# Optimization experiments

Measured on AMD Instinct MI355X. Metric: run time of the kernel, lower is better.

The kernel has to match this reference:

```python
import jax, jax.numpy as jnp
import numpy as np
import math

B, S, D, H = 4, 1024, 1024, 16
HD = D // H  # 64
DFF = 4 * D
LN_EPS = 1e-5

def setup_inputs() -> dict:
    key = jax.random.key(0)
    ks = jax.random.split(key, 24)
    sd = lambda fi, fo: 1.0 / math.sqrt(fi)
    def lin(k, fi, fo):
        k1, k2 = jax.random.split(k)
        w = jax.random.uniform(k1, (fi, fo), jnp.float32, -sd(fi, fo), sd(fi, fo))
        b = jax.random.uniform(k2, (fo,), jnp.float32, -sd(fi, fo), sd(fi, fo))
        return w, b
    x = jax.random.normal(ks[0], (B, S, D), jnp.float32)
    Wk, bk = lin(ks[1], D, D)
    Wq, bq = lin(ks[2], D, D)
    Wv, bv = lin(ks[3], D, D)
    # per-head projections stacked over heads: [H, D, HD]
    def head_lin(k):
        kk = jax.random.split(k, H)
        ws, bs = zip(*[lin(kk[h], D, HD) for h in range(H)])
        return jnp.stack(ws), jnp.stack(bs)
    Whq, bhq = head_lin(ks[4])
    Whk, bhk = head_lin(ks[5])
    Whv, bhv = head_lin(ks[6])
    Wo, bo = lin(ks[7], D, D)
    W1, b1 = lin(ks[8], D, DFF)
    W2, b2 = lin(ks[9], DFF, D)
    gamma = jnp.ones((D,), jnp.float32)
    beta = jnp.zeros((D,), jnp.float32)
    return dict(x=x, Wk=Wk, bk=bk, Wq=Wq, bq=bq, Wv=Wv, bv=bv,
                Whq=Whq, bhq=bhq, Whk=Whk, bhk=bhk, Whv=Whv, bhv=bhv,
                Wo=Wo, bo=bo, W1=W1, b1=b1, W2=W2, b2=b2,
                gamma=gamma, beta=beta)

def _layer_norm(x, gamma, beta):
    mu = jnp.mean(x, axis=-1, keepdims=True)
    var = jnp.mean(jnp.square(x - mu), axis=-1, keepdims=True)
    return (x - mu) * jax.lax.rsqrt(var + LN_EPS) * gamma + beta

def reference(x, Wk, bk, Wq, bq, Wv, bv, Whq, bhq, Whk, bhk, Whv, bhv,
              Wo, bo, W1, b1, W2, b2, gamma, beta):
    # outer projections; NOTE: forward passes (k, q, v) into MHA, so the
    # MHA 'Q' stream is k_proj(x), 'K' stream is q_proj(x), 'V' is v_proj(x)
    ko = x @ Wk + bk
    qo = x @ Wq + bq
    vo = x @ Wv + bv
    # per-head projections (batched over heads): [B,H,S,HD]
    q = jnp.einsum('bsd,hde->bhse', ko, Whq) + bhq[None, :, None, :]
    k = jnp.einsum('bsd,hde->bhse', qo, Whk) + bhk[None, :, None, :]
    v = jnp.einsum('bsd,hde->bhse', vo, Whv) + bhv[None, :, None, :]
    # NOTE: original scales by sqrt(d_model), not sqrt(head_dim)
    scores = jnp.einsum('bhse,bhte->bhst', q, k) / math.sqrt(D)
    w = jax.nn.softmax(scores, axis=-1)
    o = jnp.einsum('bhst,bhte->bhse', w, v)         # [B,H,S,HD]
    o = o.transpose(0, 2, 1, 3).reshape(B, S, D)    # concat heads
    attn = o @ Wo + bo
    # dropout is identity in eval; shared LayerNorm after both residuals
    r1 = _layer_norm(x + attn, gamma, beta)
    ff = jax.nn.gelu(r1 @ W1 + b1, approximate=False) @ W2 + b2
    out = _layer_norm(r1 + ff, gamma, beta)
    return out
```

## Files before the change

### kernel.cpp

```cpp
#include <hip/hip_runtime.h>
#include <cstdint>
#include <cstddef>

#define D_MODEL 1024
#define SEQ 1024
#define BATCH 4
#define NHEAD 16
#define HDIM 64
#define ROWS (BATCH*SEQ)

typedef unsigned short u16;
typedef __attribute__((ext_vector_type(4))) unsigned short u16x4;
typedef __attribute__((ext_vector_type(8))) unsigned short u16x8;
typedef __attribute__((ext_vector_type(8))) __bf16 bf16x8v;
typedef __attribute__((ext_vector_type(4))) float f32x4;

__device__ inline u16 f2bf(float f){
  union{float f; unsigned u;} c; c.f = f;
  unsigned r = c.u + 0x7FFFu + ((c.u>>16)&1u);
  return (u16)(r>>16);
}
__device__ inline float bf2f(u16 s){
  union{unsigned u; float f;} c; c.u = ((unsigned)s)<<16; return c.f;
}
__device__ inline float gelu_f(float x){ return 0.5f*x*(1.f+erff(x*0.7071067811865475f)); }

__device__ __forceinline__ void gload_lds16(const void* g, void* l){
  __builtin_amdgcn_global_load_lds(
    (const __attribute__((address_space(1))) unsigned int*)g,
    (__attribute__((address_space(3))) unsigned int*)l, 16, 0, 0);
}

__global__ __launch_bounds__(256) void convert_bf(const float* __restrict__ in, u16* __restrict__ out){
  size_t idx = (size_t)blockIdx.x*256 + threadIdx.x;
  f32x4 v = *(const f32x4*)(in + idx*4);
  u16x4 o = { f2bf(v.x), f2bf(v.y), f2bf(v.z), f2bf(v.w) };
  *(u16x4*)(out + idx*4) = o;
}

__global__ __launch_bounds__(256) void transpose_conv(const float* __restrict__ W, u16* __restrict__ WT, int K, int N){
  __shared__ float tile[32][33];
  int n0 = blockIdx.x*32, k0 = blockIdx.y*32;
  int tx = threadIdx.x & 31, ty = threadIdx.x >> 5;
  #pragma unroll
  for (int i=0;i<4;i++){
    int r = ty + i*8;
    tile[r][tx] = W[(size_t)(k0+r)*N + n0 + tx];
  }
  __syncthreads();
  #pragma unroll
  for (int i=0;i<4;i++){
    int r = ty + i*8;
    WT[(size_t)(n0+r)*K + k0 + tx] = f2bf(tile[tx][r]);
  }
}

__global__ __launch_bounds__(256) void head_transpose(const float* __restrict__ Wh, u16* __restrict__ WT){
  __shared__ float tile[32][33];
  int d0 = blockIdx.x*32, e0 = blockIdx.y*32, h = blockIdx.z;
  int tx = threadIdx.x & 31, ty = threadIdx.x >> 5;
  #pragma unroll
  for (int i=0;i<4;i++){
    int r = ty + i*8;
    tile[r][tx] = Wh[(size_t)h*D_MODEL*HDIM + (size_t)(d0+r)*HDIM + e0 + tx];
  }
  __syncthreads();
  #pragma unroll
  for (int i=0;i<4;i++){
    int r = ty + i*8;
    WT[(size_t)(h*HDIM + e0 + r)*D_MODEL + d0 + tx] = f2bf(tile[tx][r]);
  }
}

__device__ __forceinline__ void gemm_core(u16* As, u16* Bs,
  const u16* __restrict__ A, const u16* __restrict__ BT, const float* __restrict__ bias,
  float* __restrict__ Cf, u16* __restrict__ Cb, int N, int K, int act, int vtrans)
{
  int t = threadIdx.x;
  int lane = t & 63, wid = t >> 6;
  int wr = wid >> 1, wc = wid & 1;
  int fr = lane & 15, kg = lane >> 4;
  int tr = blockIdx.y, tc = blockIdx.x;
  const size_t Abase = (size_t)tr*128*K;
  const size_t Bbase = (size_t)tc*128*K;

  f32x4 acc[4][4];
  #pragma unroll
  for (int m=0;m<4;m++)
    #pragma unroll
    for (int n=0;n<4;n++)
      acc[m][n] = (f32x4)0.f;

  int srow = lane >> 2;
  int sch0 = lane & 3;

  for (int k0 = 0; k0 < K; k0 += 32){
    #pragma unroll
    for (int c=0;c<2;c++){
      int r0 = (wid*2 + c)*16;
      int row = r0 + srow;
      int ch = sch0 ^ ((row >> 1) & 3);
      gload_lds16(A  + Abase + (size_t)row*K + k0 + ch*8, As + r0*32);
      gload_lds16(BT + Bbase + (size_t)row*K + k0 + ch*8, Bs + r0*32);
    }
    __syncthreads();
    bf16x8v af[4], bfv[4];
    #pragma unroll
    for (int m=0;m<4;m++){
      int r = wr*64 + m*16 + fr;
      af[m] = *(const bf16x8v*)&As[r*32 + (kg ^ ((r>>1)&3))*8];
    }
    #pragma unroll
    for (int n=0;n<4;n++){
      int r = wc*64 + n*16 + fr;
      bfv[n] = *(const bf16x8v*)&Bs[r*32 + (kg ^ ((r>>1)&3))*8];
    }
    #pragma unroll
    for (int m=0;m<4;m++)
      #pragma unroll
      for (int n=0;n<4;n++)
        acc[m][n] = __builtin_amdgcn_mfma_f32_16x16x32_bf16(af[m], bfv[n], acc[m][n], 0, 0, 0);
    __syncthreads();
  }

  int crow0 = tr*128 + wr*64;
  int ccol0 = tc*128 + wc*64;
  #pragma unroll
  for (int n=0;n<4;n++){
    int col = ccol0 + n*16 + fr;
    float bv = bias[col];
    #pragma unroll
    for (int m=0;m<4;m++){
      int rbase = crow0 + m*16 + kg*4;
      #pragma unroll
      for (int i=0;i<4;i++){
        float v = acc[m][n][i] + bv;
        if (act) v = gelu_f(v);
        int row = rbase + i;
        if (Cf) Cf[(size_t)row*N + col] = v;
        if (Cb){
          if (vtrans){
            int b = row >> 10, s = row & 1023;
            int h = col >> 6,  e = col & 63;
            Cb[(((size_t)((b*NHEAD + h)*HDIM + e))<<10) + s] = f2bf(v);
          } else {
            Cb[(size_t)row*N + col] = f2bf(v);
          }
        }
      }
    }
  }
}

__global__ __launch_bounds__(256) void gemm1_kernel(
  const u16* A, const u16* BT, const float* bias, float* Cf, u16* Cb, int N, int K, int act)
{
  __shared__ __align__(16) u16 As[128*32];
  __shared__ __align__(16) u16 Bs[128*32];
  gemm_core(As, Bs, A, BT, bias, Cf, Cb, N, K, act, 0);
}

struct B3 { const u16* A[3]; const u16* BT[3]; const float* bias[3]; u16* Cb[3]; int vtrans[3]; };
__global__ __launch_bounds__(256) void gemm3_kernel(B3 p){
  __shared__ __align__(16) u16 As[128*32];
  __shared__ __align__(16) u16 Bs[128*32];
  int z = blockIdx.z;
  gemm_core(As, Bs, p.A[z], p.BT[z], p.bias[z], nullptr, p.Cb[z], D_MODEL, D_MODEL, 0, p.vtrans[z]);
}

__global__ __launch_bounds__(256) void attn_mfma(const u16* __restrict__ Q, const u16* __restrict__ Km,
                                                 const u16* __restrict__ Vt, u16* __restrict__ O)
{
  __shared__ __align__(16) u16 Ks[64*64];
  __shared__ __align__(16) u16 Vs[64*64];
  __shared__ __align__(16) u16 Ps[4][16*64];
  int t = threadIdx.x, lane = t & 63, wid = t >> 6;
  int fr = lane & 15, kg = lane >> 4;
  int qt = blockIdx.x, h = blockIdx.y, b = blockIdx.z;
  const size_t qkbase = ((size_t)b*SEQ)*D_MODEL + (size_t)h*HDIM;
  const size_t vtb = ((size_t)(b*NHEAD + h))*HDIM*SEQ;

  int qrow = qt*64 + wid*16 + fr;
  bf16x8v aq[2];
  aq[0] = *(const bf16x8v*)(Q + qkbase + (size_t)qrow*D_MODEL + kg*8);
  aq[1] = *(const bf16x8v*)(Q + qkbase + (size_t)qrow*D_MODEL + 32 + kg*8);

  f32x4 Oacc[4];
  #pragma unroll
  for (int n=0;n<4;n++) Oacc[n] = (f32x4)0.f;
  float m_run[4], l_run[4];
  #pragma unroll
  for (int i=0;i<4;i++){ m_run[i] = -3e38f; l_run[i] = 0.f; }

  int srow = lane >> 3;
  int sch  = (lane & 7) ^ srow;
  int x7 = fr & 7;

  for (int kt = 0; kt < SEQ/64; ++kt){
    #pragma unroll
    for (int c=0;c<2;c++){
      int r0 = (wid*2 + c)*8;
      int rowk = r0 + srow;
      gload_lds16(Km + qkbase + (size_t)(kt*64 + rowk)*D_MODEL + sch*8, &Ks[r0*64]);
      gload_lds16(Vt + vtb + (size_t)rowk*SEQ + kt*64 + sch*8, &Vs[r0*64]);
    }
    __syncthreads();

    f32x4 z4 = (f32x4)0.f;
    f32x4 s4[4];
    #pragma unroll
    for (int n=0;n<4;n++){
      int r = n*16 + fr;
      bf16x8v k0v = *(const bf16x8v*)&Ks[r*64 + ((kg  ) ^ x7)*8];
      bf16x8v k1v = *(const bf16x8v*)&Ks[r*64 + ((4+kg) ^ x7)*8];
      s4[n] = __builtin_amdgcn_mfma_f32_16x16x32_bf16(aq[0], k0v, z4, 0,0,0);
      s4[n] = __builtin_amdgcn_mfma_f32_16x16x32_bf16(aq[1], k1v, s4[n], 0,0,0);
      s4[n] *= 0.03125f;
    }

    float mI[4], sc[4], ls[4], p[4][4];
    #pragma unroll
    for (int i=0;i<4;i++)
      mI[i] = fmaxf(fmaxf(s4[0][i], s4[1][i]), fmaxf(s4[2][i], s4[3][i]));
    #pragma unroll
    for (int off=1; off<16; off<<=1){
      #pragma unroll
      for (int i=0;i<4;i++) mI[i] = fmaxf(mI[i], __shfl_xor(mI[i], off));
    }
    #pragma unroll
    for (int i=0;i<4;i++){
      float m_new = fmaxf(m_run[i], mI[i]);
      sc[i] = __expf(m_run[i] - m_new);
      m_run[i] = m_new;
      ls[i] = 0.f;
    }
    #pragma unroll
    for (int n=0;n<4;n++)
      #pragma unroll
      for (int i=0;i<4;i++){
        float pv = __expf(s4[n][i] - m_run[i]);
        p[n][i] = pv;
        ls[i] += pv;
      }
    #pragma unroll
    for (int off=1; off<16; off<<=1){
      #pragma unroll
      for (int i=0;i<4;i++) ls[i] += __shfl_xor(ls[i], off);
    }
    #pragma unroll
    for (int i=0;i<4;i++) l_run[i] = l_run[i]*sc[i] + ls[i];
    #pragma unroll
    for (int n=0;n<4;n++)
      #pragma unroll
      for (int i=0;i<4;i++) Oacc[n][i] *= sc[i];

    u16* Pw = &Ps[wid][0];
    #pragma unroll
    for (int n=0;n<4;n++){
      int chunk = n*2 + (fr>>3);
      #pragma unroll
      for (int i=0;i<4;i++){
        int row = kg*4 + i;
        Pw[row*64 + (chunk ^ (row&7))*8 + (fr&7)] = f2bf(p[n][i]);
      }
    }
    asm volatile("s_waitcnt lgkmcnt(0)" ::: "memory");

    bf16x8v ap0 = *(const bf16x8v*)&Pw[fr*64 + ((kg  ) ^ x7)*8];
    bf16x8v ap1 = *(const bf16x8v*)&Pw[fr*64 + ((4+kg) ^ x7)*8];
    #pragma unroll
    for (int n2=0;n2<4;n2++){
      int r = n2*16 + fr;
      bf16x8v v0 = *(const bf16x8v*)&Vs[r*64 + ((kg  ) ^ x7)*8];
      bf16x8v v1 = *(const bf16x8v*)&Vs[r*64 + ((4+kg) ^ x7)*8];
      Oacc[n2] = __builtin_amdgcn_mfma_f32_16x16x32_bf16(ap0, v0, Oacc[n2], 0,0,0);
      Oacc[n2] = __builtin_amdgcn_mfma_f32_16x16x32_bf16(ap1, v1, Oacc[n2], 0,0,0);
    }
    __syncthreads();
  }

  float inv[4];
  #pragma unroll
  for (int i=0;i<4;i++) inv[i] = 1.f / l_run[i];
  #pragma unroll
  for (int n2=0;n2<4;n2++){
    #pragma unroll
    for (int i=0;i<4;i++){
      int row = qt*64 + wid*16 + kg*4 + i;
      O[qkbase + (size_t)row*D_MODEL + n2*16 + fr] = f2bf(Oacc[n2][i]*inv[i]);
    }
  }
}

__global__ __launch_bounds__(256) void ln_kernel(const float* __restrict__ A, const float* __restrict__ B,
   const float* __restrict__ gamma, const float* __restrict__ beta,
   float* __restrict__ Of, u16* __restrict__ Ob)
{
  int row = blockIdx.x, t = threadIdx.x;
  size_t base = (size_t)row*D_MODEL + t*4;
  f32x4 av = *(const f32x4*)(A + base);
  f32x4 bv = *(const f32x4*)(B + base);
  f32x4 v = av + bv;
  float s = v.x+v.y+v.z+v.w;
  float q = v.x*v.x+v.y*v.y+v.z*v.z+v.w*v.w;
  #pragma unroll
  for (int off=1; off<64; off<<=1){ s += __shfl_xor(s,off); q += __shfl_xor(q,off); }
  __shared__ float red[8];
  int wid = t>>6;
  if ((t&63)==0){ red[wid] = s; red[wid+4] = q; }
  __syncthreads();
  s = red[0]+red[1]+red[2]+red[3];
  q = red[4]+red[5]+red[6]+red[7];
  float mu = s*(1.f/1024.f);
  float var = q*(1.f/1024.f) - mu*mu;
  float rs = rsqrtf(var + 1e-5f);
  f32x4 g4 = *(const f32x4*)(gamma + t*4);
  f32x4 b4 = *(const f32x4*)(beta + t*4);
  f32x4 o;
  o.x = (v.x-mu)*rs*g4.x + b4.x;
  o.y = (v.y-mu)*rs*g4.y + b4.y;
  o.z = (v.z-mu)*rs*g4.z + b4.z;
  o.w = (v.w-mu)*rs*g4.w + b4.w;
  *(f32x4*)(Of + base) = o;
  if (Ob){
    u16x4 ob = { f2bf(o.x), f2bf(o.y), f2bf(o.z), f2bf(o.w) };
    *(u16x4*)(Ob + base) = ob;
  }
}

extern "C" void kernel_launch(void* const* d_in, const int* in_sizes, int n_in,
                              void* d_out, int out_size, void* d_ws, size_t ws_size,
                              hipStream_t stream)
{
  const float* x    = (const float*)d_in[0];
  const float* Wk   = (const float*)d_in[1];
  const float* bk   = (const float*)d_in[2];
  const float* Wq   = (const float*)d_in[3];
  const float* bq   = (const float*)d_in[4];
  const float* Wv   = (const float*)d_in[5];
  const float* bv   = (const float*)d_in[6];
  const float* Whq  = (const float*)d_in[7];
  const float* bhq  = (const float*)d_in[8];
  const float* Whk  = (const float*)d_in[9];
  const float* bhk  = (const float*)d_in[10];
  const float* Whv  = (const float*)d_in[11];
  const float* bhv  = (const float*)d_in[12];
  const float* Wo   = (const float*)d_in[13];
  const float* bo   = (const float*)d_in[14];
  const float* W1   = (const float*)d_in[15];
  const float* b1   = (const float*)d_in[16];
  const float* W2   = (const float*)d_in[17];
  const float* b2   = (const float*)d_in[18];
  const float* gamma= (const float*)d_in[19];
  const float* beta = (const float*)d_in[20];

  char* ws = (char*)d_ws;
  const size_t MB_ = 1024*1024;
  u16* WkT  = (u16*)(ws + 0*MB_);
  u16* WqT  = (u16*)(ws + 2*MB_);
  u16* WvT  = (u16*)(ws + 4*MB_);
  u16* WhqT = (u16*)(ws + 6*MB_);
  u16* WhkT = (u16*)(ws + 8*MB_);
  u16* WhvT = (u16*)(ws + 10*MB_);
  u16* WoT  = (u16*)(ws + 12*MB_);
  u16* W1T  = (u16*)(ws + 14*MB_);
  u16* W2T  = (u16*)(ws + 22*MB_);
  u16* xb   = (u16*)(ws + 30*MB_);
  u16* kob  = (u16*)(ws + 38*MB_);
  u16* qob  = (u16*)(ws + 46*MB_);
  u16* vob  = (u16*)(ws + 54*MB_);
  u16* qb   = (u16*)(ws + 62*MB_);
  u16* kb   = (u16*)(ws + 70*MB_);
  u16* vt   = (u16*)(ws + 78*MB_);
  u16* Ob   = (u16*)(ws + 86*MB_);
  float* attn_f = (float*)(ws + 94*MB_);
  float* r1f    = (float*)(ws + 110*MB_);
  u16*  r1b     = (u16*)(ws + 126*MB_);
  u16*  ff1b    = (u16*)(ws + 38*MB_);
  float* ff2f   = (float*)(ws + 94*MB_);

  dim3 tb(256);

  convert_bf<<<dim3(ROWS*D_MODEL/4/256), tb, 0, stream>>>(x, xb);
  transpose_conv<<<dim3(32,32),  tb, 0, stream>>>(Wk, WkT, 1024, 1024);
  transpose_conv<<<dim3(32,32),  tb, 0, stream>>>(Wq, WqT, 1024, 1024);
  transpose_conv<<<dim3(32,32),  tb, 0, stream>>>(Wv, WvT, 1024, 1024);
  transpose_conv<<<dim3(32,32),  tb, 0, stream>>>(Wo, WoT, 1024, 1024);
  transpose_conv<<<dim3(128,32), tb, 0, stream>>>(W1, W1T, 1024, 4096);
  transpose_conv<<<dim3(32,128), tb, 0, stream>>>(W2, W2T, 4096, 1024);
  head_transpose<<<dim3(32,2,16), tb, 0, stream>>>(Whq, WhqT);
  head_transpose<<<dim3(32,2,16), tb, 0, stream>>>(Whk, WhkT);
  head_transpose<<<dim3(32,2,16), tb, 0, stream>>>(Whv, WhvT);

  B3 p1;
  p1.A[0]=xb;  p1.A[1]=xb;  p1.A[2]=xb;
  p1.BT[0]=WkT; p1.BT[1]=WqT; p1.BT[2]=WvT;
  p1.bias[0]=bk; p1.bias[1]=bq; p1.bias[2]=bv;
  p1.Cb[0]=kob; p1.Cb[1]=qob; p1.Cb[2]=vob;
  p1.vtrans[0]=0; p1.vtrans[1]=0; p1.vtrans[2]=0;
  gemm3_kernel<<<dim3(8,32,3), tb, 0, stream>>>(p1);

  B3 p2;
  p2.A[0]=kob; p2.A[1]=qob; p2.A[2]=vob;
  p2.BT[0]=WhqT; p2.BT[1]=WhkT; p2.BT[2]=WhvT;
  p2.bias[0]=bhq; p2.bias[1]=bhk; p2.bias[2]=bhv;
  p2.Cb[0]=qb; p2.Cb[1]=kb; p2.Cb[2]=vt;
  p2.vtrans[0]=0; p2.vtrans[1]=0; p2.vtrans[2]=1;
  gemm3_kernel<<<dim3(8,32,3), tb, 0, stream>>>(p2);

  attn_mfma<<<dim3(16,16,4), tb, 0, stream>>>(qb, kb, vt, Ob);

  gemm1_kernel<<<dim3(8,32), tb, 0, stream>>>(Ob, WoT, bo, attn_f, nullptr, 1024, 1024, 0);
  ln_kernel<<<dim3(4096), tb, 0, stream>>>(x, attn_f, gamma, beta, r1f, r1b);
  gemm1_kernel<<<dim3(32,32), tb, 0, stream>>>(r1b, W1T, b1, nullptr, ff1b, 4096, 1024, 1);
  gemm1_kernel<<<dim3(8,32), tb, 0, stream>>>(ff1b, W2T, b2, ff2f, nullptr, 1024, 4096, 0);
  ln_kernel<<<dim3(4096), tb, 0, stream>>>(r1f, ff2f, gamma, beta, (float*)d_out, nullptr);

  (void)in_sizes; (void)n_in; (void)out_size; (void)ws_size;
}
```

Measured before the change: 376.6 us.

## Triple-buffer GEMM staging, fuse QKV projection, split-K output GEMMs into LayerNorm

```diff
diff --git a/kernel.cpp b/kernel.cpp
--- a/kernel.cpp
+++ b/kernel.cpp
@@ -72,55 +72,90 @@
   }
 }
 
-__device__ __forceinline__ void gemm_core(u16* As, u16* Bs,
+__global__ __launch_bounds__(256) void bias_cat(const float* a, const float* b, const float* c, float* o){
+  int i = blockIdx.x*256 + threadIdx.x;
+  float v = (i < 1024) ? a[i] : (i < 2048) ? b[i-1024] : c[i-2048];
+  o[i] = v;
+}
+
+__device__ __forceinline__ void stage128(u16 (*As)[4096], u16 (*Bs)[4096], int b,
+  const u16* Ab, const u16* Bb, int Kstride, int kt, int wid, int rr, int sch)
+{
+  #pragma unroll
+  for (int c=0;c<2;c++){
+    int reg = c*4 + wid;
+    int row = reg*16 + rr;
+    gload_lds16(Ab + (size_t)row*Kstride + kt*32 + sch*8, &As[b][reg*512]);
+  }
+  #pragma unroll
+  for (int c=0;c<2;c++){
+    int reg = c*4 + wid;
+    int row = reg*16 + rr;
+    gload_lds16(Bb + (size_t)row*Kstride + kt*32 + sch*8, &Bs[b][reg*512]);
+  }
+}
+
+__device__ __forceinline__ void gemm128_core(u16 (*As)[4096], u16 (*Bs)[4096],
   const u16* __restrict__ A, const u16* __restrict__ BT, const float* __restrict__ bias,
-  float* __restrict__ Cf, u16* __restrict__ Cb, int N, int K, int act, int vtrans)
-{
-  int t = threadIdx.x;
-  int lane = t & 63, wid = t >> 6;
-  int wr = wid >> 1, wc = wid & 1;
-  int fr = lane & 15, kg = lane >> 4;
-  int tr = blockIdx.y, tc = blockIdx.x;
-  const size_t Abase = (size_t)tr*128*K;
-  const size_t Bbase = (size_t)tc*128*K;
+  float* __restrict__ outF, u16* __restrict__ outB,
+  int N, int Kstride, int kofs, int Ksub, int mode, int act, int addbias)
+{
+  int t = threadIdx.x, lane = t&63, wid = t>>6;
+  int wr = wid>>1, wc = wid&1;
+  int fr = lane&15, kg = lane>>4;
+  int gx = gridDim.x;
+  int bid = blockIdx.y*gx + blockIdx.x;
+  int nwg = gx*gridDim.y;
+  int cpx = nwg >> 3;
+  int sw = (bid&7)*cpx + (bid>>3);
+  int tc = sw % gx, tr = sw / gx;
+
+  const u16* Ab = A  + (size_t)tr*128*Kstride + kofs;
+  const u16* Bb = BT + (size_t)tc*128*Kstride + kofs;
+  int rr = lane>>2, cc = lane&3;
+  int sch = cc ^ ((rr>>1)&3);
 
   f32x4 acc[4][4];
   #pragma unroll
   for (int m=0;m<4;m++)
     #pragma unroll
-    for (int n=0;n<4;n++)
-      acc[m][n] = (f32x4)0.f;
-
-  int srow = lane >> 2;
-  int sch0 = lane & 3;
-
-  for (int k0 = 0; k0 < K; k0 += 32){
-    #pragma unroll
-    for (int c=0;c<2;c++){
-      int r0 = (wid*2 + c)*16;
-      int row = r0 + srow;
-      int ch = sch0 ^ ((row >> 1) & 3);
-      gload_lds16(A  + Abase + (size_t)row*K + k0 + ch*8, As + r0*32);
-      gload_lds16(BT + Bbase + (size_t)row*K + k0 + ch*8, Bs + r0*32);
-    }
-    __syncthreads();
+    for (int n=0;n<4;n++) acc[m][n] = (f32x4)0.f;
+
+  int NT = Ksub >> 5;
+
+  stage128(As, Bs, 0, Ab, Bb, Kstride, 0, wid, rr, sch);
+  stage128(As, Bs, 1, Ab, Bb, Kstride, 1, wid, rr, sch);
+  int buf = 0;
+  for (int kt=0; kt<NT; ++kt){
+    if (kt+2 < NT){
+      int nb = buf+2; if (nb>=3) nb-=3;
+      stage128(As, Bs, nb, Ab, Bb, Kstride, kt+2, wid, rr, sch);
+      asm volatile("s_waitcnt vmcnt(8)" ::: "memory");
+    } else if (kt+1 < NT){
+      asm volatile("s_waitcnt vmcnt(4)" ::: "memory");
+    } else {
+      asm volatile("s_waitcnt vmcnt(0)" ::: "memory");
+    }
+    asm volatile("s_barrier" ::: "memory");
     bf16x8v af[4], bfv[4];
     #pragma unroll
     for (int m=0;m<4;m++){
       int r = wr*64 + m*16 + fr;
-      af[m] = *(const bf16x8v*)&As[r*32 + (kg ^ ((r>>1)&3))*8];
+      af[m] = *(const bf16x8v*)&As[buf][r*32 + (kg ^ ((r>>1)&3))*8];
     }
     #pragma unroll
     for (int n=0;n<4;n++){
       int r = wc*64 + n*16 + fr;
-      bfv[n] = *(const bf16x8v*)&Bs[r*32 + (kg ^ ((r>>1)&3))*8];
+      bfv[n] = *(const bf16x8v*)&Bs[buf][r*32 + (kg ^ ((r>>1)&3))*8];
     }
     #pragma unroll
     for (int m=0;m<4;m++)
       #pragma unroll
       for (int n=0;n<4;n++)
-        acc[m][n] = __builtin_amdgcn_mfma_f32_16x16x32_bf16(af[m], bfv[n], acc[m][n], 0, 0, 0);
-    __syncthreads();
+        acc[m][n] = __builtin_amdgcn_mfma_f32_16x16x32_bf16(af[m], bfv[n], acc[m][n], 0,0,0);
+    if (kt+1 < NT)
+      asm volatile("s_barrier" ::: "memory");
+    buf += 1; if (buf >= 3) buf = 0;
   }
 
   int crow0 = tr*128 + wr*64;
@@ -128,7 +163,7 @@
   #pragma unroll
   for (int n=0;n<4;n++){
     int col = ccol0 + n*16 + fr;
-    float bv = bias[col];
+    float bv = addbias ? bias[col] : 0.f;
     #pragma unroll
     for (int m=0;m<4;m++){
       int rbase = crow0 + m*16 + kg*4;
@@ -137,35 +172,49 @@
         float v = acc[m][n][i] + bv;
         if (act) v = gelu_f(v);
         int row = rbase + i;
-        if (Cf) Cf[(size_t)row*N + col] = v;
-        if (Cb){
-          if (vtrans){
-            int b = row >> 10, s = row & 1023;
-            int h = col >> 6,  e = col & 63;
-            Cb[(((size_t)((b*NHEAD + h)*HDIM + e))<<10) + s] = f2bf(v);
-          } else {
-            Cb[(size_t)row*N + col] = f2bf(v);
-          }
+        if (mode == 0){
+          outB[(size_t)(col>>10)*((size_t)ROWS*1024) + (size_t)row*1024 + (col&1023)] = f2bf(v);
+        } else if (mode == 1){
+          outB[(size_t)row*N + col] = f2bf(v);
+        } else if (mode == 2){
+          int b = row >> 10, s = row & 1023;
+          int h = col >> 6, e = col & 63;
+          outB[(((size_t)((b*NHEAD + h)*HDIM + e))<<10) + s] = f2bf(v);
+        } else {
+          outF[(size_t)row*1024 + col] = v;
         }
       }
     }
   }
 }
 
-__global__ __launch_bounds__(256) void gemm1_kernel(
-  const u16* A, const u16* BT, const float* bias, float* Cf, u16* Cb, int N, int K, int act)
-{
-  __shared__ __align__(16) u16 As[128*32];
-  __shared__ __align__(16) u16 Bs[128*32];
-  gemm_core(As, Bs, A, BT, bias, Cf, Cb, N, K, act, 0);
-}
-
-struct B3 { const u16* A[3]; const u16* BT[3]; const float* bias[3]; u16* Cb[3]; int vtrans[3]; };
-__global__ __launch_bounds__(256) void gemm3_kernel(B3 p){
-  __shared__ __align__(16) u16 As[128*32];
-  __shared__ __align__(16) u16 Bs[128*32];
+__global__ __launch_bounds__(256) void g_gemm(
+  const u16* A, const u16* BT, const float* bias, float* outF, u16* outB,
+  int N, int K, int mode, int act)
+{
+  __shared__ __align__(16) u16 As[3][4096];
+  __shared__ __align__(16) u16 Bs[3][4096];
+  gemm128_core(As, Bs, A, BT, bias, outF, outB, N, K, 0, K, mode, act, 1);
+}
+
+__global__ __launch_bounds__(256) void g_gemm_sk(
+  const u16* A, const u16* BT, const float* bias, float* outBase, int K)
+{
+  __shared__ __align__(16) u16 As[3][4096];
+  __shared__ __align__(16) u16 Bs[3][4096];
   int z = blockIdx.z;
-  gemm_core(As, Bs, p.A[z], p.BT[z], p.bias[z], nullptr, p.Cb[z], D_MODEL, D_MODEL, 0, p.vtrans[z]);
+  int Ksub = K >> 1;
+  gemm128_core(As, Bs, A, BT, bias, outBase + (size_t)z*ROWS*1024, nullptr,
+               1024, K, z*Ksub, Ksub, 3, 0, z==0);
+}
+
+struct B3 { const u16* A[3]; const u16* BT[3]; const float* bias[3]; u16* Cb[3]; int mode[3]; };
+__global__ __launch_bounds__(256) void g_gemm_b3(B3 p){
+  __shared__ __align__(16) u16 As[3][4096];
+  __shared__ __align__(16) u16 Bs[3][4096];
+  int z = blockIdx.z;
+  gemm128_core(As, Bs, p.A[z], p.BT[z], p.bias[z], nullptr, p.Cb[z],
+               1024, 1024, 0, 1024, p.mode[z], 0, 1);
 }
 
 __global__ __launch_bounds__(256) void attn_mfma(const u16* __restrict__ Q, const u16* __restrict__ Km,
@@ -292,15 +341,15 @@
   }
 }
 
-__global__ __launch_bounds__(256) void ln_kernel(const float* __restrict__ A, const float* __restrict__ B,
-   const float* __restrict__ gamma, const float* __restrict__ beta,
+__global__ __launch_bounds__(256) void ln_sum3(const float* __restrict__ A, const float* __restrict__ B,
+   const float* __restrict__ C, const float* __restrict__ gamma, const float* __restrict__ beta,
    float* __restrict__ Of, u16* __restrict__ Ob)
 {
   int row = blockIdx.x, t = threadIdx.x;
   size_t base = (size_t)row*D_MODEL + t*4;
-  f32x4 av = *(const f32x4*)(A + base);
-  f32x4 bv = *(const f32x4*)(B + base);
-  f32x4 v = av + bv;
+  f32x4 v = *(const f32x4*)(A + base);
+  v += *(const f32x4*)(B + base);
+  v += *(const f32x4*)(C + base);
   float s = v.x+v.y+v.z+v.w;
   float q = v.x*v.x+v.y*v.y+v.z*v.z+v.w*v.w;
   #pragma unroll
@@ -321,7 +370,7 @@
   o.y = (v.y-mu)*rs*g4.y + b4.y;
   o.z = (v.z-mu)*rs*g4.z + b4.z;
   o.w = (v.w-mu)*rs*g4.w + b4.w;
-  *(f32x4*)(Of + base) = o;
+  if (Of) *(f32x4*)(Of + base) = o;
   if (Ob){
     u16x4 ob = { f2bf(o.x), f2bf(o.y), f2bf(o.z), f2bf(o.w) };
     *(u16x4*)(Ob + base) = ob;
@@ -373,11 +422,12 @@
   u16* kb   = (u16*)(ws + 70*MB_);
   u16* vt   = (u16*)(ws + 78*MB_);
   u16* Ob   = (u16*)(ws + 86*MB_);
-  float* attn_f = (float*)(ws + 94*MB_);
-  float* r1f    = (float*)(ws + 110*MB_);
-  u16*  r1b     = (u16*)(ws + 126*MB_);
-  u16*  ff1b    = (u16*)(ws + 38*MB_);
-  float* ff2f   = (float*)(ws + 94*MB_);
+  u16* ff1b = (u16*)(ws + 38*MB_);
+  float* r1f = (float*)(ws + 70*MB_);
+  u16*  r1b  = (u16*)(ws + 86*MB_);
+  float* P0  = (float*)(ws + 94*MB_);
+  float* P1  = (float*)(ws + 110*MB_);
+  float* bcat = (float*)(ws + 126*MB_);
 
   dim3 tb(256);
 
@@ -391,30 +441,25 @@
   head_transpose<<<dim3(32,2,16), tb, 0, stream>>>(Whq, WhqT);
   head_transpose<<<dim3(32,2,16), tb, 0, stream>>>(Whk, WhkT);
   head_transpose<<<dim3(32,2,16), tb, 0, stream>>>(Whv, WhvT);
-
-  B3 p1;
-  p1.A[0]=xb;  p1.A[1]=xb;  p1.A[2]=xb;
-  p1.BT[0]=WkT; p1.BT[1]=WqT; p1.BT[2]=WvT;
-  p1.bias[0]=bk; p1.bias[1]=bq; p1.bias[2]=bv;
-  p1.Cb[0]=kob; p1.Cb[1]=qob; p1.Cb[2]=vob;
-  p1.vtrans[0]=0; p1.vtrans[1]=0; p1.vtrans[2]=0;
-  gemm3_kernel<<<dim3(8,32,3), tb, 0, stream>>>(p1);
+  bias_cat<<<dim3(12), tb, 0, stream>>>(bk, bq, bv, bcat);
+
+  g_gemm<<<dim3(24,32), tb, 0, stream>>>(xb, WkT, bcat, nullptr, kob, 3072, 1024, 0, 0);
 
   B3 p2;
   p2.A[0]=kob; p2.A[1]=qob; p2.A[2]=vob;
   p2.BT[0]=WhqT; p2.BT[1]=WhkT; p2.BT[2]=WhvT;
   p2.bias[0]=bhq; p2.bias[1]=bhk; p2.bias[2]=bhv;
   p2.Cb[0]=qb; p2.Cb[1]=kb; p2.Cb[2]=vt;
-  p2.vtrans[0]=0; p2.vtrans[1]=0; p2.vtrans[2]=1;
-  gemm3_kernel<<<dim3(8,32,3), tb, 0, stream>>>(p2);
+  p2.mode[0]=1; p2.mode[1]=1; p2.mode[2]=2;
+  g_gemm_b3<<<dim3(8,32,3), tb, 0, stream>>>(p2);
 
   attn_mfma<<<dim3(16,16,4), tb, 0, stream>>>(qb, kb, vt, Ob);
 
-  gemm1_kernel<<<dim3(8,32), tb, 0, stream>>>(Ob, WoT, bo, attn_f, nullptr, 1024, 1024, 0);
-  ln_kernel<<<dim3(4096), tb, 0, stream>>>(x, attn_f, gamma, beta, r1f, r1b);
-  gemm1_kernel<<<dim3(32,32), tb, 0, stream>>>(r1b, W1T, b1, nullptr, ff1b, 4096, 1024, 1);
-  gemm1_kernel<<<dim3(8,32), tb, 0, stream>>>(ff1b, W2T, b2, ff2f, nullptr, 1024, 4096, 0);
-  ln_kernel<<<dim3(4096), tb, 0, stream>>>(r1f, ff2f, gamma, beta, (float*)d_out, nullptr);
+  g_gemm_sk<<<dim3(8,32,2), tb, 0, stream>>>(Ob, WoT, bo, P0, 1024);
+  ln_sum3<<<dim3(4096), tb, 0, stream>>>(x, P0, P1, gamma, beta, r1f, r1b);
+  g_gemm<<<dim3(32,32), tb, 0, stream>>>(r1b, W1T, b1, nullptr, ff1b, 4096, 1024, 1, 1);
+  g_gemm_sk<<<dim3(8,32,2), tb, 0, stream>>>(ff1b, W2T, b2, P0, 4096);
+  ln_sum3<<<dim3(4096), tb, 0, stream>>>(r1f, P0, P1, gamma, beta, (float*)d_out, nullptr);
 
   (void)in_sizes; (void)n_in; (void)out_size; (void)ws_size;
 }
```

Result: faster. 353.2 us (-6.2%).
